# Performance work log

Hardware: AMD Instinct MI355X
Metric: run time of the kernel (lower is better)

Reference implementation:

```python
import jax, jax.numpy as jnp
import numpy as np

EPS = 1e-6  # clamp epsilon in GeM
NORM_EPS = 1e-12  # torch F.normalize eps
PATCH_SIZES = (3,)


def l2norm(x, axis):
    n = jnp.sqrt(jnp.sum(x * x, axis=axis, keepdims=True))
    return x / jnp.maximum(n, NORM_EPS)


def setup_inputs() -> dict:
    key = jax.random.key(0)
    k1, k2, k3 = jax.random.split(key, 3)
    N, D, H, W, F = 16, 2048, 32, 32, 512
    x = jax.random.normal(k1, (N, D, H, W), jnp.float32)
    proj_w = jax.random.normal(k2, (F, D), jnp.float32) * (1.0 / np.sqrt(D))
    proj_b = jax.random.normal(k3, (F,), jnp.float32) * 0.01
    p = jnp.full((1,), 3.0, jnp.float32)
    return {"x": x, "proj_w": proj_w, "proj_b": proj_b, "p": p}


def reference(x, proj_w, proj_b, p):
    # ---- GeM global descriptor (global_pool path inside local_pool) ----
    x = l2norm(x, axis=1)                                  # L2 over channel dim
    g = jnp.clip(x, EPS, None) ** p[0]                     # [N,D,H,W]
    g = g.mean(axis=(-2, -1))                              # [N,D]
    g = g ** (1.0 / p[0])
    g = g @ proj_w.T + proj_b                              # [N,F]
    g = l2norm(g, axis=1)

    # ---- integral image over spatial dims ----
    integ = jnp.cumsum(jnp.cumsum(x, axis=-1), axis=-2)    # [N,D,H,W]

    local_descs = []
    for ps in PATCH_SIZES:
        off = ps // 2
        # zero-pad (1+off) on top/left, then replicate-pad off on bottom/right
        ipad = jnp.pad(integ, ((0, 0), (0, 0), (1 + off, 0), (1 + off, 0)))
        ipad = jnp.pad(ipad, ((0, 0), (0, 0), (0, off), (0, off)), mode='edge')
        # box sum via 4-corner integral-image difference
        # == grouped 2x2 conv with dilation=ps, weights [[1,-1],[-1,1]], stride=1
        box = (ipad[:, :, :-ps, :-ps] - ipad[:, :, :-ps, ps:]
               - ipad[:, :, ps:, :-ps] + ipad[:, :, ps:, ps:])  # [N,D,H,W]
        N, D, Hh, Ww = box.shape
        pd = box.reshape(N, D, Hh * Ww).transpose(0, 2, 1)  # [N,HW,D]
        pd = pd @ proj_w.T + proj_b                         # [N,HW,F]
        pd = l2norm(pd, axis=2)
        local_descs.append(pd.transpose(0, 2, 1))           # [N,F,HW]

    return g, local_descs[0]
```

## Files before the change

kernel.cpp:

```cpp
#include <hip/hip_runtime.h>
#include <hip/hip_bf16.h>

#define N_ 16
#define D_ 2048
#define H_ 32
#define W_ 32
#define HW_ 1024
#define F_ 512

typedef unsigned short u16;
typedef unsigned int u32;
typedef __attribute__((ext_vector_type(8))) short bf16x8;
typedef __attribute__((ext_vector_type(4))) float f32x4;

__device__ __forceinline__ u16 f2bf(float f) {
  __hip_bfloat16 h = __float2bfloat16(f);
  union { __hip_bfloat16 h; u16 u; } c; c.h = h;
  return c.u;
}

__global__ __launch_bounds__(256) void k_zero(float* __restrict__ p) {
  int i = blockIdx.x * 256 + threadIdx.x;
  ((float4*)p)[i] = (float4){0.f, 0.f, 0.f, 0.f};
}

__global__ __launch_bounds__(256) void k_sumsq(const float* __restrict__ x, float* __restrict__ sumsq) {
  const int n = blockIdx.x;
  const int dc = blockIdx.y;
  const int t = threadIdx.x;
  const float* xp = x + ((size_t)n * D_ + (size_t)dc * 64) * HW_;
  float s0 = 0.f, s1 = 0.f, s2 = 0.f, s3 = 0.f;
  for (int d = 0; d < 64; ++d) {
    const float* row = xp + (size_t)d * HW_;
    float v0 = row[t], v1 = row[t + 256], v2 = row[t + 512], v3 = row[t + 768];
    s0 += v0 * v0; s1 += v1 * v1; s2 += v2 * v2; s3 += v3 * v3;
  }
  atomicAdd(&sumsq[n * HW_ + t      ], s0);
  atomicAdd(&sumsq[n * HW_ + t + 256], s1);
  atomicAdd(&sumsq[n * HW_ + t + 512], s2);
  atomicAdd(&sumsq[n * HW_ + t + 768], s3);
}

__global__ __launch_bounds__(256) void k_wconv(const float* __restrict__ w, u16* __restrict__ packB) {
  const int i = blockIdx.x * 256 + threadIdx.x;
  const int lane = i & 63, nf = (i >> 6) & 3, kt = (i >> 8) & 63, wq = i >> 14;
  const int r15 = lane & 15, hi = lane >> 4;
  const int f = wq * 64 + nf * 16 + r15;
  const int k = kt * 32 + hi * 8;
  const float* src = w + (size_t)f * D_ + k;
  float4 v0 = *(const float4*)(src);
  float4 v1 = *(const float4*)(src + 4);
  u16 r[8] = { f2bf(v0.x), f2bf(v0.y), f2bf(v0.z), f2bf(v0.w),
               f2bf(v1.x), f2bf(v1.y), f2bf(v1.z), f2bf(v1.w) };
  *(uint4*)(packB + (size_t)i * 8) = *(const uint4*)r;
}

__global__ __launch_bounds__(512) void k_boxgemm(const float* __restrict__ x,
    const float* __restrict__ sumsq, const float* __restrict__ pvec,
    const u16* __restrict__ packB, const float* __restrict__ bias,
    float* __restrict__ gbuf, float* __restrict__ outL) {
  const int mt = blockIdx.x;
  const int n  = mt >> 4;
  const int hA = (mt & 15) * 2;
  const int hw0 = (mt & 15) * 64;
  const int t = threadIdx.x;
  const int lane = t & 63, wv = t >> 6;
  const int r15 = lane & 15, hi = lane >> 4;
  const int hp2 = t >> 8;
  const int dd = (t & 255) >> 3;
  const int w4 = t & 7, wq = w4 * 4;
  const float p = pvec[0];
  const bool p3c = (p == 3.0f);

  __shared__ __align__(16) float smem[128 * 68];
  float* hs = smem;
  u16*   Af = (u16*)(smem + 4608);
  float* rnl = smem + 4608 + 1024;
  __shared__ float s_sq[8][64];
  __shared__ float s_rn[64];

  if (t < 128) {
    int jj = t >> 5, w = t & 31;
    int hp = hA - 1 + jj;
    float r = 0.f;
    if (hp >= 0 && hp < H_) r = 1.0f / fmaxf(sqrtf(sumsq[n * HW_ + hp * W_ + w]), 1e-12f);
    rnl[jj * 32 + w] = r;
  }
  __syncthreads();

  f32x4 acc[4][4];
  #pragma unroll
  for (int a = 0; a < 4; ++a)
    #pragma unroll
    for (int b = 0; b < 4; ++b) acc[a][b] = (f32x4){0.f, 0.f, 0.f, 0.f};

  const int hpa0 = hA - 1 + hp2;
  const int hpa1 = hA + 1 + hp2;
  const bool val0 = (hpa0 >= 0);
  const bool val1 = (hpa1 < H_);
  const float* xb0 = x + ((size_t)(n * D_ + dd) * HW_ + (val0 ? hpa0 : 0) * W_ + wq);
  const float* xb1 = x + ((size_t)(n * D_ + dd) * HW_ + (val1 ? hpa1 : 0) * W_ + wq);
  const int hsoff0 = hp2 * 1152 + dd * 36 + wq;
  const int hsoff1 = (hp2 + 2) * 1152 + dd * 36 + wq;
  const float4 zero4 = {0.f, 0.f, 0.f, 0.f};

  const u16* bbase = packB + (size_t)wv * 131072 + lane * 8;

  float4 xa0 = val0 ? *(const float4*)(xb0) : zero4;
  float4 xa1 = val1 ? *(const float4*)(xb1) : zero4;
  bf16x8 bc[4], bn[4];
  #pragma unroll
  for (int nf = 0; nf < 4; ++nf) bc[nf] = *(const bf16x8*)(bbase + nf * 512);

  for (int kt = 0; kt < 64; ++kt) {
    float4 xn0, xn1;
    if (kt < 63) {
      const size_t xoff = (size_t)(kt + 1) * 32 * HW_;
      xn0 = val0 ? *(const float4*)(xb0 + xoff) : zero4;
      xn1 = val1 ? *(const float4*)(xb1 + xoff) : zero4;
      #pragma unroll
      for (int nf = 0; nf < 4; ++nf)
        bn[nf] = *(const bf16x8*)(bbase + ((size_t)(kt + 1) * 4 + nf) * 512);
    }

    float4 rr0 = *(const float4*)(rnl + hp2 * 32 + wq);
    float4 rr1 = *(const float4*)(rnl + (hp2 + 2) * 32 + wq);
    float4 v0, v1;
    v0.x = xa0.x * rr0.x; v0.y = xa0.y * rr0.y; v0.z = xa0.z * rr0.z; v0.w = xa0.w * rr0.w;
    v1.x = xa1.x * rr1.x; v1.y = xa1.y * rr1.y; v1.z = xa1.z * rr1.z; v1.w = xa1.w * rr1.w;
    {
      float4 pk = hp2 ? v0 : v1;
      float cx = fmaxf(pk.x, 1e-6f), cy = fmaxf(pk.y, 1e-6f);
      float cz = fmaxf(pk.z, 1e-6f), cw = fmaxf(pk.w, 1e-6f);
      float g;
      if (p3c) g = cx * cx * cx + cy * cy * cy + cz * cz * cz + cw * cw * cw;
      else     g = __powf(cx, p) + __powf(cy, p) + __powf(cz, p) + __powf(cw, p);
      g += __shfl_xor(g, 1, 8);
      g += __shfl_xor(g, 2, 8);
      g += __shfl_xor(g, 4, 8);
      if (w4 == 0) atomicAdd(&gbuf[n * D_ + kt * 32 + dd], g);
    }
    {
      float lf = __shfl_up(v0.w, 1, 8), rf = __shfl_down(v0.x, 1, 8);
      if (w4 == 0) lf = 0.f;
      if (w4 == 7) rf = 0.f;
      float4 h;
      h.x = lf + v0.x + v0.y;  h.y = v0.x + v0.y + v0.z;
      h.z = v0.y + v0.z + v0.w; h.w = v0.z + v0.w + rf;
      *(float4*)(hs + hsoff0) = h;
    }
    {
      float lf = __shfl_up(v1.w, 1, 8), rf = __shfl_down(v1.x, 1, 8);
      if (w4 == 0) lf = 0.f;
      if (w4 == 7) rf = 0.f;
      float4 h;
      h.x = lf + v1.x + v1.y;  h.y = v1.x + v1.y + v1.z;
      h.z = v1.y + v1.z + v1.w; h.w = v1.z + v1.w + rf;
      *(float4*)(hs + hsoff1) = h;
    }
    __syncthreads();

    {
      const float* hb = hs + hp2 * 1152 + dd * 36 + wq;
      float4 h0 = *(const float4*)(hb);
      float4 h1 = *(const float4*)(hb + 1152);
      float4 h2 = *(const float4*)(hb + 2304);
      float o[4] = { h0.x + h1.x + h2.x, h0.y + h1.y + h2.y,
                     h0.z + h1.z + h2.z, h0.w + h1.w + h2.w };
      const int hii = dd >> 3, jj = dd & 7;
      #pragma unroll
      for (int i = 0; i < 4; ++i) {
        int r = hp2 * 32 + wq + i;
        Af[(r >> 4) * 512 + hii * 128 + (r & 15) * 8 + jj] = f2bf(o[i]);
      }
    }
    __syncthreads();

    bf16x8 af[4];
    #pragma unroll
    for (int mf = 0; mf < 4; ++mf)
      af[mf] = *(const bf16x8*)(Af + mf * 512 + lane * 8);
    #pragma unroll
    for (int mf = 0; mf < 4; ++mf)
      #pragma unroll
      for (int nf = 0; nf < 4; ++nf)
        acc[mf][nf] = __builtin_amdgcn_mfma_f32_16x16x32_bf16(af[mf], bc[nf], acc[mf][nf], 0, 0, 0);

    xa0 = xn0; xa1 = xn1;
    #pragma unroll
    for (int nf = 0; nf < 4; ++nf) bc[nf] = bn[nf];
  }

  __syncthreads();
  float badd[4];
  #pragma unroll
  for (int nf = 0; nf < 4; ++nf) badd[nf] = bias[wv * 64 + nf * 16 + r15];
  #pragma unroll
  for (int mf = 0; mf < 4; ++mf)
    #pragma unroll
    for (int nf = 0; nf < 4; ++nf)
      #pragma unroll
      for (int j = 0; j < 4; ++j) acc[mf][nf][j] += badd[nf];

  #pragma unroll
  for (int mf = 0; mf < 4; ++mf)
    #pragma unroll
    for (int j = 0; j < 4; ++j) {
      float s = 0.f;
      #pragma unroll
      for (int nf = 0; nf < 4; ++nf) { float v = acc[mf][nf][j]; s += v * v; }
      s += __shfl_xor(s, 1); s += __shfl_xor(s, 2); s += __shfl_xor(s, 4); s += __shfl_xor(s, 8);
      if ((lane & 15) == 0) s_sq[wv][mf * 16 + hi * 4 + j] = s;
    }
  __syncthreads();
  if (t < 64) {
    float s = 0.f;
    #pragma unroll
    for (int w8 = 0; w8 < 8; ++w8) s += s_sq[w8][t];
    s_rn[t] = 1.0f / fmaxf(sqrtf(s), 1e-12f);
  }
  __syncthreads();

  float* ct = smem;
  for (int nf = 0; nf < 4; ++nf) {
    const int fi = wv * 16 + r15;
    #pragma unroll
    for (int mf = 0; mf < 4; ++mf)
      #pragma unroll
      for (int j = 0; j < 4; ++j) {
        int m = mf * 16 + hi * 4 + j;
        ct[fi * 68 + m] = acc[mf][nf][j] * s_rn[m];
      }
    __syncthreads();
    {
      int fr = t >> 2, mq = t & 3;
      int f = (fr >> 4) * 64 + nf * 16 + (fr & 15);
      float* dst = outL + ((size_t)(n * F_ + f)) * HW_ + hw0 + mq * 16;
      const float* srcp = ct + fr * 68 + mq * 16;
      float4 a0 = *(const float4*)(srcp);
      float4 a1 = *(const float4*)(srcp + 4);
      float4 a2 = *(const float4*)(srcp + 8);
      float4 a3 = *(const float4*)(srcp + 12);
      *(float4*)(dst) = a0; *(float4*)(dst + 4) = a1;
      *(float4*)(dst + 8) = a2; *(float4*)(dst + 12) = a3;
    }
    __syncthreads();
  }
}

__global__ __launch_bounds__(256) void k_gem_fin(const float* __restrict__ gbuf,
    const float* __restrict__ pvec, float* __restrict__ gg) {
  int i = blockIdx.x * 256 + threadIdx.x;
  float p = pvec[0];
  float m = gbuf[i] * (1.0f / 1024.0f);
  gg[i] = (p == 3.0f) ? cbrtf(m) : powf(m, 1.0f / p);
}

__global__ __launch_bounds__(256) void k_gproj(const float* __restrict__ w,
    const float* __restrict__ bias, const float* __restrict__ gg,
    float* __restrict__ gproj) {
  const int f = blockIdx.x;
  const int t = threadIdx.x;
  float wreg[8];
  #pragma unroll
  for (int j = 0; j < 8; ++j) wreg[j] = w[(size_t)f * D_ + t + j * 256];
  __shared__ float red[4];
  const int lane = t & 63, wv = t >> 6;
  for (int n = 0; n < N_; ++n) {
    float s = 0.f;
    #pragma unroll
    for (int j = 0; j < 8; ++j) s += wreg[j] * gg[n * D_ + t + j * 256];
    #pragma unroll
    for (int off = 32; off >= 1; off >>= 1) s += __shfl_down(s, off);
    if (lane == 0) red[wv] = s;
    __syncthreads();
    if (t == 0) gproj[n * F_ + f] = red[0] + red[1] + red[2] + red[3] + bias[f];
    __syncthreads();
  }
}

__global__ __launch_bounds__(512) void k_gnorm(const float* __restrict__ gproj, float* __restrict__ outg) {
  const int n = blockIdx.x;
  const int t = threadIdx.x;
  float v = gproj[n * F_ + t];
  float s = v * v;
  const int lane = t & 63, wv = t >> 6;
  #pragma unroll
  for (int off = 32; off >= 1; off >>= 1) s += __shfl_down(s, off);
  __shared__ float red[8];
  __shared__ float rtot;
  if (lane == 0) red[wv] = s;
  __syncthreads();
  if (t == 0) {
    float a = 0.f;
    #pragma unroll
    for (int i = 0; i < 8; ++i) a += red[i];
    rtot = 1.0f / fmaxf(sqrtf(a), 1e-12f);
  }
  __syncthreads();
  outg[n * F_ + t] = v * rtot;
}

extern "C" void kernel_launch(void* const* d_in, const int* in_sizes, int n_in,
                              void* d_out, int out_size, void* d_ws, size_t ws_size,
                              hipStream_t stream) {
  const float* x  = (const float*)d_in[0];
  const float* pw = (const float*)d_in[1];
  const float* pb = (const float*)d_in[2];
  const float* pv = (const float*)d_in[3];
  float* out = (float*)d_out;

  char* ws = (char*)d_ws;
  float* sumsq = (float*)ws;
  float* gbuf  = (float*)(ws + 65536);
  float* gg    = (float*)(ws + 65536 + 131072);
  float* gproj = (float*)(ws + 65536 + 2 * 131072);
  u16*   packB = (u16*)(ws + 65536 + 2 * 131072 + 32768);

  k_zero<<<dim3(48), dim3(256), 0, stream>>>(sumsq);
  k_sumsq<<<dim3(16, 32), dim3(256), 0, stream>>>(x, sumsq);
  k_wconv<<<dim3(512), dim3(256), 0, stream>>>(pw, packB);
  k_boxgemm<<<dim3(256), dim3(512), 0, stream>>>(x, sumsq, pv, packB, pb, gbuf, out + N_ * F_);
  k_gem_fin<<<dim3(128), dim3(256), 0, stream>>>(gbuf, pv, gg);
  k_gproj<<<dim3(512), dim3(256), 0, stream>>>(pw, pb, gg, gproj);
  k_gnorm<<<dim3(16), dim3(512), 0, stream>>>(gproj, out);
}
```

Before: 141.0 us.

## Compute box filter in registers with double-buffered A tile, one barrier per step

The 3x3 box filter now runs on 256 threads entirely in registers: each thread loads three input rows for two channels, so the vertical sum no longer goes through a shared-memory staging buffer. The A tile in LDS is double-buffered, and the producer threads build tile kt+1 while all waves run MFMAs on tile kt, which cuts the loop to one __syncthreads per step instead of two. Stores to LDS are packed as pairs of bf16. In exchange, the producer threads load three times as many global rows, carry extra registers for the two-deep prefetch, and leave half the block idle during box computation.

Result: slower. 196.1 us (+39.1%).

```diff
diff --git a/kernel.cpp b/kernel.cpp
--- a/kernel.cpp
+++ b/kernel.cpp
@@ -17,6 +17,9 @@
   __hip_bfloat16 h = __float2bfloat16(f);
   union { __hip_bfloat16 h; u16 u; } c; c.h = h;
   return c.u;
+}
+__device__ __forceinline__ u32 f2bf2(float lo, float hi) {
+  return (u32)f2bf(lo) | ((u32)f2bf(hi) << 16);
 }
 
 __global__ __launch_bounds__(256) void k_zero(float* __restrict__ p) {
@@ -61,21 +64,25 @@
     float* __restrict__ gbuf, float* __restrict__ outL) {
   const int mt = blockIdx.x;
   const int n  = mt >> 4;
-  const int hA = (mt & 15) * 2;
-  const int hw0 = (mt & 15) * 64;
+  const int hseg = mt & 15;
+  const int hA = hseg * 2;
+  const int hw0 = hseg * 64;
   const int t = threadIdx.x;
   const int lane = t & 63, wv = t >> 6;
   const int r15 = lane & 15, hi = lane >> 4;
-  const int hp2 = t >> 8;
-  const int dd = (t & 255) >> 3;
-  const int w4 = t & 7, wq = w4 * 4;
   const float p = pvec[0];
   const bool p3c = (p == 3.0f);
 
+  const bool bxt = (t < 256);
+  const int dp = t >> 4;
+  const int w4 = (t >> 1) & 7;
+  const int rh = t & 1;
+  const int wq = w4 * 4;
+  const int h_out = hA + rh;
+
   __shared__ __align__(16) float smem[128 * 68];
-  float* hs = smem;
-  u16*   Af = (u16*)(smem + 4608);
-  float* rnl = smem + 4608 + 1024;
+  u16* Af = (u16*)smem;
+  float* rnl = smem + 2048;
   __shared__ float s_sq[8][64];
   __shared__ float s_rn[64];
 
@@ -86,7 +93,6 @@
     if (hp >= 0 && hp < H_) r = 1.0f / fmaxf(sqrtf(sumsq[n * HW_ + hp * W_ + w]), 1e-12f);
     rnl[jj * 32 + w] = r;
   }
-  __syncthreads();
 
   f32x4 acc[4][4];
   #pragma unroll
@@ -94,104 +100,128 @@
     #pragma unroll
     for (int b = 0; b < 4; ++b) acc[a][b] = (f32x4){0.f, 0.f, 0.f, 0.f};
 
-  const int hpa0 = hA - 1 + hp2;
-  const int hpa1 = hA + 1 + hp2;
-  const bool val0 = (hpa0 >= 0);
-  const bool val1 = (hpa1 < H_);
-  const float* xb0 = x + ((size_t)(n * D_ + dd) * HW_ + (val0 ? hpa0 : 0) * W_ + wq);
-  const float* xb1 = x + ((size_t)(n * D_ + dd) * HW_ + (val1 ? hpa1 : 0) * W_ + wq);
-  const int hsoff0 = hp2 * 1152 + dd * 36 + wq;
-  const int hsoff1 = (hp2 + 2) * 1152 + dd * 36 + wq;
   const float4 zero4 = {0.f, 0.f, 0.f, 0.f};
+  const int hr0 = h_out - 1, hr2 = h_out + 1;
+  const bool v0ok = (hr0 >= 0), v2ok = (hr2 < H_);
+  const float* xp0 = x + ((size_t)(n * D_ + 2 * dp)) * HW_ + (v0ok ? hr0 : 0) * W_ + wq;
+  const float* xp1 = x + ((size_t)(n * D_ + 2 * dp)) * HW_ + h_out * W_ + wq;
+  const float* xp2 = x + ((size_t)(n * D_ + 2 * dp)) * HW_ + (v2ok ? hr2 : 0) * W_ + wq;
+
+  float4 xa[6], xn[6];
+  auto loadx = [&](int kt, float4* X) {
+    size_t o = (size_t)kt * 32 * HW_;
+    X[0] = v0ok ? *(const float4*)(xp0 + o) : zero4;
+    X[1] = v0ok ? *(const float4*)(xp0 + o + HW_) : zero4;
+    X[2] = *(const float4*)(xp1 + o);
+    X[3] = *(const float4*)(xp1 + o + HW_);
+    X[4] = v2ok ? *(const float4*)(xp2 + o) : zero4;
+    X[5] = v2ok ? *(const float4*)(xp2 + o + HW_) : zero4;
+  };
+  auto boxc = [&](int kt, float4* X) {
+    float4 rn0 = *(const float4*)(rnl + rh * 32 + wq);
+    float4 rn1 = *(const float4*)(rnl + (rh + 1) * 32 + wq);
+    float4 rn2 = *(const float4*)(rnl + (rh + 2) * 32 + wq);
+    float4 ve[2][3];
+    #pragma unroll
+    for (int e = 0; e < 2; ++e) {
+      ve[e][0].x = X[e].x * rn0.x;     ve[e][0].y = X[e].y * rn0.y;
+      ve[e][0].z = X[e].z * rn0.z;     ve[e][0].w = X[e].w * rn0.w;
+      ve[e][1].x = X[2 + e].x * rn1.x; ve[e][1].y = X[2 + e].y * rn1.y;
+      ve[e][1].z = X[2 + e].z * rn1.z; ve[e][1].w = X[2 + e].w * rn1.w;
+      ve[e][2].x = X[4 + e].x * rn2.x; ve[e][2].y = X[4 + e].y * rn2.y;
+      ve[e][2].z = X[4 + e].z * rn2.z; ve[e][2].w = X[4 + e].w * rn2.w;
+    }
+    float g[2];
+    #pragma unroll
+    for (int e = 0; e < 2; ++e) {
+      float cx = fmaxf(ve[e][1].x, 1e-6f), cy = fmaxf(ve[e][1].y, 1e-6f);
+      float cz = fmaxf(ve[e][1].z, 1e-6f), cw = fmaxf(ve[e][1].w, 1e-6f);
+      if (p3c) g[e] = cx * cx * cx + cy * cy * cy + cz * cz * cz + cw * cw * cw;
+      else     g[e] = __powf(cx, p) + __powf(cy, p) + __powf(cz, p) + __powf(cw, p);
+    }
+    #pragma unroll
+    for (int e = 0; e < 2; ++e) {
+      g[e] += __shfl_xor(g[e], 1, 16);
+      g[e] += __shfl_xor(g[e], 2, 16);
+      g[e] += __shfl_xor(g[e], 4, 16);
+      g[e] += __shfl_xor(g[e], 8, 16);
+    }
+    if ((lane & 15) == 0) {
+      atomicAdd(&gbuf[n * D_ + kt * 32 + 2 * dp    ], g[0]);
+      atomicAdd(&gbuf[n * D_ + kt * 32 + 2 * dp + 1], g[1]);
+    }
+    float4 o[2];
+    #pragma unroll
+    for (int e = 0; e < 2; ++e) {
+      float4 h[3];
+      #pragma unroll
+      for (int k = 0; k < 3; ++k) {
+        float lf = __shfl_up(ve[e][k].w, 2, 16);
+        float rf = __shfl_down(ve[e][k].x, 2, 16);
+        if (w4 == 0) lf = 0.f;
+        if (w4 == 7) rf = 0.f;
+        h[k].x = lf + ve[e][k].x + ve[e][k].y;
+        h[k].y = ve[e][k].x + ve[e][k].y + ve[e][k].z;
+        h[k].z = ve[e][k].y + ve[e][k].z + ve[e][k].w;
+        h[k].w = ve[e][k].z + ve[e][k].w + rf;
+      }
+      o[e].x = h[0].x + h[1].x + h[2].x;
+      o[e].y = h[0].y + h[1].y + h[2].y;
+      o[e].z = h[0].z + h[1].z + h[2].z;
+      o[e].w = h[0].w + h[1].w + h[2].w;
+    }
+    u32* d32 = (u32*)(Af + (kt & 1) * 2048);
+    const float oe[4] = {o[0].x, o[0].y, o[0].z, o[0].w};
+    const float oo[4] = {o[1].x, o[1].y, o[1].z, o[1].w};
+    #pragma unroll
+    for (int i = 0; i < 4; ++i) {
+      int r = rh * 32 + wq + i;
+      d32[(r >> 4) * 256 + (dp >> 2) * 64 + (r & 15) * 4 + (dp & 3)] = f2bf2(oe[i], oo[i]);
+    }
+  };
 
   const u16* bbase = packB + (size_t)wv * 131072 + lane * 8;
-
-  float4 xa0 = val0 ? *(const float4*)(xb0) : zero4;
-  float4 xa1 = val1 ? *(const float4*)(xb1) : zero4;
   bf16x8 bc[4], bn[4];
   #pragma unroll
   for (int nf = 0; nf < 4; ++nf) bc[nf] = *(const bf16x8*)(bbase + nf * 512);
 
+  __syncthreads();
+  if (bxt) {
+    loadx(0, xa);
+    boxc(0, xa);
+    loadx(1, xa);
+  }
+  __syncthreads();
+
   for (int kt = 0; kt < 64; ++kt) {
-    float4 xn0, xn1;
-    if (kt < 63) {
-      const size_t xoff = (size_t)(kt + 1) * 32 * HW_;
-      xn0 = val0 ? *(const float4*)(xb0 + xoff) : zero4;
-      xn1 = val1 ? *(const float4*)(xb1 + xoff) : zero4;
+    if (kt + 1 < 64) {
       #pragma unroll
       for (int nf = 0; nf < 4; ++nf)
         bn[nf] = *(const bf16x8*)(bbase + ((size_t)(kt + 1) * 4 + nf) * 512);
     }
-
-    float4 rr0 = *(const float4*)(rnl + hp2 * 32 + wq);
-    float4 rr1 = *(const float4*)(rnl + (hp2 + 2) * 32 + wq);
-    float4 v0, v1;
-    v0.x = xa0.x * rr0.x; v0.y = xa0.y * rr0.y; v0.z = xa0.z * rr0.z; v0.w = xa0.w * rr0.w;
-    v1.x = xa1.x * rr1.x; v1.y = xa1.y * rr1.y; v1.z = xa1.z * rr1.z; v1.w = xa1.w * rr1.w;
-    {
-      float4 pk = hp2 ? v0 : v1;
-      float cx = fmaxf(pk.x, 1e-6f), cy = fmaxf(pk.y, 1e-6f);
-      float cz = fmaxf(pk.z, 1e-6f), cw = fmaxf(pk.w, 1e-6f);
-      float g;
-      if (p3c) g = cx * cx * cx + cy * cy * cy + cz * cz * cz + cw * cw * cw;
-      else     g = __powf(cx, p) + __powf(cy, p) + __powf(cz, p) + __powf(cw, p);
-      g += __shfl_xor(g, 1, 8);
-      g += __shfl_xor(g, 2, 8);
-      g += __shfl_xor(g, 4, 8);
-      if (w4 == 0) atomicAdd(&gbuf[n * D_ + kt * 32 + dd], g);
-    }
-    {
-      float lf = __shfl_up(v0.w, 1, 8), rf = __shfl_down(v0.x, 1, 8);
-      if (w4 == 0) lf = 0.f;
-      if (w4 == 7) rf = 0.f;
-      float4 h;
-      h.x = lf + v0.x + v0.y;  h.y = v0.x + v0.y + v0.z;
-      h.z = v0.y + v0.z + v0.w; h.w = v0.z + v0.w + rf;
-      *(float4*)(hs + hsoff0) = h;
-    }
-    {
-      float lf = __shfl_up(v1.w, 1, 8), rf = __shfl_down(v1.x, 1, 8);
-      if (w4 == 0) lf = 0.f;
-      if (w4 == 7) rf = 0.f;
-      float4 h;
-      h.x = lf + v1.x + v1.y;  h.y = v1.x + v1.y + v1.z;
-      h.z = v1.y + v1.z + v1.w; h.w = v1.z + v1.w + rf;
-      *(float4*)(hs + hsoff1) = h;
-    }
-    __syncthreads();
-
-    {
-      const float* hb = hs + hp2 * 1152 + dd * 36 + wq;
-      float4 h0 = *(const float4*)(hb);
-      float4 h1 = *(const float4*)(hb + 1152);
-      float4 h2 = *(const float4*)(hb + 2304);
-      float o[4] = { h0.x + h1.x + h2.x, h0.y + h1.y + h2.y,
-                     h0.z + h1.z + h2.z, h0.w + h1.w + h2.w };
-      const int hii = dd >> 3, jj = dd & 7;
-      #pragma unroll
-      for (int i = 0; i < 4; ++i) {
-        int r = hp2 * 32 + wq + i;
-        Af[(r >> 4) * 512 + hii * 128 + (r & 15) * 8 + jj] = f2bf(o[i]);
-      }
-    }
-    __syncthreads();
-
+    if (bxt && kt + 2 < 64) loadx(kt + 2, xn);
+    if (bxt && kt + 1 < 64) boxc(kt + 1, xa);
+
+    const u16* Ar = Af + (kt & 1) * 2048;
     bf16x8 af[4];
     #pragma unroll
     for (int mf = 0; mf < 4; ++mf)
-      af[mf] = *(const bf16x8*)(Af + mf * 512 + lane * 8);
+      af[mf] = *(const bf16x8*)(Ar + mf * 512 + lane * 8);
     #pragma unroll
     for (int mf = 0; mf < 4; ++mf)
       #pragma unroll
       for (int nf = 0; nf < 4; ++nf)
         acc[mf][nf] = __builtin_amdgcn_mfma_f32_16x16x32_bf16(af[mf], bc[nf], acc[mf][nf], 0, 0, 0);
 
-    xa0 = xn0; xa1 = xn1;
+    if (bxt) {
+      #pragma unroll
+      for (int q = 0; q < 6; ++q) xa[q] = xn[q];
+    }
     #pragma unroll
     for (int nf = 0; nf < 4; ++nf) bc[nf] = bn[nf];
-  }
-
-  __syncthreads();
+    __syncthreads();
+  }
+
   float badd[4];
   #pragma unroll
   for (int nf = 0; nf < 4; ++nf) badd[nf] = bias[wv * 64 + nf * 16 + r15];
```
